# Kernel tuning notes

Measured on AMD Instinct MI355X. Metric: run time of the kernel, lower is better.

Reference implementation:

```python
import jax, jax.numpy as jnp
import numpy as np

CDIM = 256  # part_size for energy_pooling_mask


def setup_inputs() -> dict:
    key = jax.random.key(0)
    ks = jax.random.split(key, 6)
    B, T, IDIM, HDIM, ODIM = 8, 2048, 512, 2048, 512
    x = jax.random.normal(ks[0], (B, T, IDIM), dtype=jnp.float32)
    mask_prev = jax.random.randint(ks[1], (B, T, HDIM), 0, 2, dtype=jnp.int32)
    W_enc = jax.random.normal(ks[2], (HDIM, IDIM), dtype=jnp.float32) * 0.02
    b_enc = jax.random.normal(ks[3], (HDIM,), dtype=jnp.float32) * 0.02
    W_dec = jax.random.normal(ks[4], (ODIM, HDIM), dtype=jnp.float32) * 0.02
    b_dec = jax.random.normal(ks[5], (ODIM,), dtype=jnp.float32) * 0.02
    return {"x": x, "mask_prev": mask_prev, "W_enc": W_enc, "b_enc": b_enc,
            "W_dec": W_dec, "b_dec": b_dec}


def _energy_pooling_mask(h, part_size):
    # topk over channel (last) dim of h^2; share=True -> k = 2*part_size
    B, T, H = h.shape
    k2 = 2 * part_size
    _, idx = jax.lax.top_k(h * h, k2)            # [B, T, 2c] unique indices
    idx_f = idx.reshape(B * T, k2)
    rows = jnp.arange(B * T)[:, None]
    base = jnp.zeros((B * T, H), dtype=h.dtype)
    # sum of one-hots over unique indices == scatter-set of 1.0
    mask_share = base.at[rows, idx_f].set(1.0).reshape(B, T, H)
    mask_cur = base.at[rows, idx_f[:, :part_size]].set(1.0).reshape(B, T, H)
    return mask_cur, mask_share


def reference(x, mask_prev, W_enc, b_enc, W_dec, b_dec):
    # encoder: Linear(idim -> hdim)
    h = jnp.einsum('bti,hi->bth', x, W_enc) + b_enc
    # hidden_exclude_activation with mask_prev given:
    # h[mask_prev.bool()] = 0
    mp = mask_prev.astype(h.dtype)
    h = jnp.where(mp > 0, jnp.zeros((), h.dtype), h)
    mask_cur, mask_cur_share = _energy_pooling_mask(h, CDIM)
    mask_prev_new = mp + mask_cur
    # h.masked_fill(~mask_cur_share.bool(), 0)
    h = h * mask_cur_share
    # decoder_src: Linear(hdim -> odim)
    out = jnp.einsum('bth,oh->bto', h, W_dec) + b_dec
    return out, mask_prev_new
```

## Files before the change

### kernel.cpp

```cpp
#include <hip/hip_runtime.h>
#include <hip/hip_bf16.h>

typedef __attribute__((ext_vector_type(8))) __bf16 bf16x8;
typedef __attribute__((ext_vector_type(4))) float f32x4;

#define MDIM 16384
#define HDIM 2048
#define IDIM 512
#define ODIM 512
#define CAP 768

static __device__ __forceinline__ unsigned short f2bf(float f) {
  unsigned int u = __float_as_uint(f);
  unsigned int r = (u + 0x7fffu + ((u >> 16) & 1u)) >> 16;
  return (unsigned short)r;
}

__global__ void cvt_bf16_kernel(const float* __restrict__ src,
                                unsigned short* __restrict__ dst, int n) {
  int i = (blockIdx.x * 256 + threadIdx.x) * 4;
  if (i >= n) return;
  float4 v = *(const float4*)(src + i);
  unsigned int a = (unsigned int)f2bf(v.x) | ((unsigned int)f2bf(v.y) << 16);
  unsigned int b = (unsigned int)f2bf(v.z) | ((unsigned int)f2bf(v.w) << 16);
  uint2 st; st.x = a; st.y = b;
  *(uint2*)(dst + i) = st;
}

__global__ __launch_bounds__(256) void gemm1_kernel(
    const float* __restrict__ x,
    const float* __restrict__ wenc,
    const float* __restrict__ benc,
    float* __restrict__ h) {
  __shared__ __align__(16) float As[32][132];
  __shared__ __align__(16) float Bs[32][132];
  const int t = threadIdx.x;
  const int tx = t & 15, ty = t >> 4;
  const int m0 = blockIdx.y * 128;
  const int n0 = blockIdx.x * 128;
  const int r0 = t >> 1;
  const int kh = (t & 1) * 16;

  const float* pa = x + (size_t)(m0 + r0) * IDIM + kh;
  const float* pb = wenc + (size_t)(n0 + r0) * IDIM + kh;

  float acc[8][8];
#pragma unroll
  for (int i = 0; i < 8; ++i)
#pragma unroll
    for (int j = 0; j < 8; ++j) acc[i][j] = 0.f;

  for (int kt = 0; kt < IDIM; kt += 32) {
    float4 a0 = *(const float4*)(pa + kt);
    float4 a1 = *(const float4*)(pa + kt + 4);
    float4 a2 = *(const float4*)(pa + kt + 8);
    float4 a3 = *(const float4*)(pa + kt + 12);
    float4 b0 = *(const float4*)(pb + kt);
    float4 b1 = *(const float4*)(pb + kt + 4);
    float4 b2 = *(const float4*)(pb + kt + 8);
    float4 b3 = *(const float4*)(pb + kt + 12);
    __syncthreads();
    {
      const float* aa = (const float*)&a0;
      const float av[16] = {a0.x, a0.y, a0.z, a0.w, a1.x, a1.y, a1.z, a1.w,
                            a2.x, a2.y, a2.z, a2.w, a3.x, a3.y, a3.z, a3.w};
      const float bv[16] = {b0.x, b0.y, b0.z, b0.w, b1.x, b1.y, b1.z, b1.w,
                            b2.x, b2.y, b2.z, b2.w, b3.x, b3.y, b3.z, b3.w};
      (void)aa;
#pragma unroll
      for (int j = 0; j < 16; ++j) {
        As[kh + j][r0] = av[j];
        Bs[kh + j][r0] = bv[j];
      }
    }
    __syncthreads();
#pragma unroll
    for (int k = 0; k < 32; ++k) {
      float4 av0 = *(const float4*)&As[k][ty * 4];
      float4 av1 = *(const float4*)&As[k][64 + ty * 4];
      float4 bv0 = *(const float4*)&Bs[k][tx * 4];
      float4 bv1 = *(const float4*)&Bs[k][64 + tx * 4];
      float am[8] = {av0.x, av0.y, av0.z, av0.w, av1.x, av1.y, av1.z, av1.w};
      float bm[8] = {bv0.x, bv0.y, bv0.z, bv0.w, bv1.x, bv1.y, bv1.z, bv1.w};
#pragma unroll
      for (int i = 0; i < 8; ++i)
#pragma unroll
        for (int j = 0; j < 8; ++j) acc[i][j] += am[i] * bm[j];
    }
  }
  float4 be0 = *(const float4*)(benc + n0 + tx * 4);
  float4 be1 = *(const float4*)(benc + n0 + 64 + tx * 4);
  float bb[8] = {be0.x, be0.y, be0.z, be0.w, be1.x, be1.y, be1.z, be1.w};
#pragma unroll
  for (int i = 0; i < 8; ++i) {
    int m = m0 + ((i < 4) ? (ty * 4 + i) : (64 + ty * 4 + (i - 4)));
    float* hrow = h + (size_t)m * HDIM + n0;
    float4 s0 = {acc[i][0] + bb[0], acc[i][1] + bb[1], acc[i][2] + bb[2], acc[i][3] + bb[3]};
    float4 s1 = {acc[i][4] + bb[4], acc[i][5] + bb[5], acc[i][6] + bb[6], acc[i][7] + bb[7]};
    *(float4*)(hrow + tx * 4) = s0;
    *(float4*)(hrow + 64 + tx * 4) = s1;
  }
}

__global__ __launch_bounds__(256) void select_kernel(
    float* __restrict__ hbuf,
    const int* __restrict__ maskp,
    unsigned short* __restrict__ hs) {
  const int row = blockIdx.x;
  const int t = threadIdx.x;
  const int lane = t & 63;
  const int w = t >> 6;
  __shared__ int hist[4096];
  __shared__ unsigned int cand512[CAP];
  __shared__ unsigned int cand256[CAP];
  __shared__ int scal[16];
  __shared__ int n512, n256;

  float* hrow = hbuf + (size_t)row * HDIM;
  const int* mrow = maskp + (size_t)row * HDIM;
  float hv[8];
  *(float4*)&hv[0] = *(const float4*)(hrow + t * 8);
  *(float4*)&hv[4] = *(const float4*)(hrow + t * 8 + 4);
  int4 mp0 = *(const int4*)(mrow + t * 8);
  int4 mp1 = *(const int4*)(mrow + t * 8 + 4);
  int mm[8] = {mp0.x, mp0.y, mp0.z, mp0.w, mp1.x, mp1.y, mp1.z, mp1.w};
#pragma unroll
  for (int i = 0; i < 8; ++i) hv[i] = (mm[i] > 0) ? 0.f : hv[i];
  unsigned int key[8];
#pragma unroll
  for (int i = 0; i < 8; ++i) key[i] = __float_as_uint(hv[i] * hv[i]);

#pragma unroll
  for (int i = 0; i < 16; ++i) hist[t + i * 256] = 0;
  if (t == 0) {
    n512 = 0; n256 = 0;
    scal[0] = 0; scal[1] = 0x40000000;
    scal[2] = 0; scal[3] = 0x40000000;
  }
  __syncthreads();
#pragma unroll
  for (int i = 0; i < 8; ++i)
    if (key[i]) atomicAdd(&hist[key[i] >> 20], 1);
  __syncthreads();

  if (w == 0) {
    const int base = lane * 64;
    int s = 0;
#pragma unroll
    for (int i = 0; i < 64; i += 4) {
      int4 hh = *(const int4*)&hist[base + i];
      s += hh.x + hh.y + hh.z + hh.w;
    }
    int rs = s;
#pragma unroll
    for (int d = 1; d < 64; d <<= 1) {
      int o = __shfl_down(rs, d, 64);
      rs += (lane + d < 64) ? o : 0;
    }
    int c = rs - s;
    for (int i = 60; i >= 0; i -= 4) {
      int4 hh = *(const int4*)&hist[base + i];
      int q[4] = {hh.x, hh.y, hh.z, hh.w};
#pragma unroll
      for (int j = 3; j >= 0; --j) {
        int hc = q[j];
        if (c < 512 && c + hc >= 512) { scal[0] = base + i + j; scal[1] = 512 - c; }
        if (c < 256 && c + hc >= 256) { scal[2] = base + i + j; scal[3] = 256 - c; }
        c += hc;
      }
    }
  }
  __syncthreads();
  const int b512 = scal[0], b256 = scal[2];
#pragma unroll
  for (int i = 0; i < 8; ++i) {
    if (key[i]) {
      int bin = (int)(key[i] >> 20);
      if (bin == b512) { int p = atomicAdd(&n512, 1); if (p < CAP) cand512[p] = key[i]; }
      if (bin == b256) { int p = atomicAdd(&n256, 1); if (p < CAP) cand256[p] = key[i]; }
    }
  }
  __syncthreads();

  if (w < 2) {
    const unsigned int bb = (unsigned int)scal[w * 2];
    const int r = scal[w * 2 + 1];
    const unsigned int* cand = w ? cand256 : cand512;
    int C = w ? n256 : n512;
    C = (C < CAP) ? C : CAP;
    unsigned int v = 0;
    if (r <= C) {
      v = bb << 20;
      for (int bit = 19; bit >= 0; --bit) {
        unsigned int cth = v | (1u << bit);
        int cnt = 0;
        for (int p = lane; p < C; p += 64) cnt += (cand[p] >= cth) ? 1 : 0;
#pragma unroll
        for (int d = 1; d < 64; d <<= 1) cnt += __shfl_xor(cnt, d, 64);
        if (cnt >= r) v = cth;
      }
    }
    if (lane == 0) scal[4 + w] = (int)v;
  }
  __syncthreads();
  const unsigned int v512 = (unsigned int)scal[4];
  const unsigned int v256 = (unsigned int)scal[5];

  int g = 0;
#pragma unroll
  for (int i = 0; i < 8; ++i) {
    g += (key[i] > v512) ? 1 : 0;
    g += (key[i] > v256) ? (1 << 16) : 0;
  }
#pragma unroll
  for (int d = 1; d < 64; d <<= 1) g += __shfl_xor(g, d, 64);
  if (lane == 0) scal[8 + w] = g;
  __syncthreads();
  g = scal[8] + scal[9] + scal[10] + scal[11];
  const int r512 = 512 - (g & 0xffff);
  const int r256 = 256 - (g >> 16);

  int tc = 0;
#pragma unroll
  for (int i = 0; i < 8; ++i) {
    tc += (key[i] == v512) ? 1 : 0;
    tc += (key[i] == v256) ? (1 << 16) : 0;
  }
  int sc = tc;
#pragma unroll
  for (int d = 1; d < 64; d <<= 1) {
    int o = __shfl_up(sc, d, 64);
    if (lane >= d) sc += o;
  }
  if (lane == 63) scal[12 + w] = sc;
  __syncthreads();
  int excl = sc - tc;
  for (int i = 0; i < w; ++i) excl += scal[12 + i];
  int run512 = excl & 0xffff;
  int run256 = (excl >> 16) & 0xffff;

  float mpn[8];
  unsigned int hb[4];
#pragma unroll
  for (int i = 0; i < 8; ++i) {
    bool share, cur;
    if (key[i] > v512) share = true;
    else if (key[i] == v512) { share = (run512 < r512); run512++; }
    else share = false;
    if (key[i] > v256) cur = true;
    else if (key[i] == v256) { cur = (run256 < r256); run256++; }
    else cur = false;
    mpn[i] = (float)mm[i] + (cur ? 1.0f : 0.0f);
    unsigned short bbits = f2bf(share ? hv[i] : 0.0f);
    if (i & 1) hb[i >> 1] |= ((unsigned int)bbits << 16);
    else hb[i >> 1] = (unsigned int)bbits;
  }
  float4 s0 = {mpn[0], mpn[1], mpn[2], mpn[3]};
  float4 s1 = {mpn[4], mpn[5], mpn[6], mpn[7]};
  *(float4*)(hrow + t * 8) = s0;
  *(float4*)(hrow + t * 8 + 4) = s1;
  uint4 hstore = {hb[0], hb[1], hb[2], hb[3]};
  *(uint4*)(hs + (size_t)row * HDIM + t * 8) = hstore;
}

__global__ __launch_bounds__(256) void gemm2_kernel(
    const unsigned short* __restrict__ A,
    const unsigned short* __restrict__ B,
    const float* __restrict__ bdec,
    float* __restrict__ out) {
  __shared__ __align__(16) __bf16 As[64 * 32];
  __shared__ __align__(16) __bf16 Bs[128 * 32];
  const int t = threadIdx.x;
  const int lane = t & 63;
  const int w = t >> 6;
  const int wm = w >> 1, wn = w & 1;
  const int m0 = blockIdx.y * 64;
  const int n0 = blockIdx.x * 128;
  const int r = t >> 2;
  const int k8 = (t & 3) * 8;

  f32x4 acc[2][4];
#pragma unroll
  for (int i = 0; i < 2; ++i)
#pragma unroll
    for (int j = 0; j < 4; ++j) acc[i][j] = (f32x4){0.f, 0.f, 0.f, 0.f};

  const int la = lane & 15;
  const int kq = (lane >> 4) * 8;

  for (int kt = 0; kt < HDIM; kt += 32) {
    uint4 a0 = *(const uint4*)(A + (size_t)(m0 + r) * HDIM + kt + k8);
    uint4 b0 = *(const uint4*)(B + (size_t)(n0 + r) * HDIM + kt + k8);
    uint4 b1 = *(const uint4*)(B + (size_t)(n0 + 64 + r) * HDIM + kt + k8);
    __syncthreads();
    *(uint4*)&As[r * 32 + k8] = a0;
    *(uint4*)&Bs[r * 32 + k8] = b0;
    *(uint4*)&Bs[(64 + r) * 32 + k8] = b1;
    __syncthreads();
    bf16x8 af[2], bg[4];
#pragma unroll
    for (int mi = 0; mi < 2; ++mi)
      af[mi] = *(const bf16x8*)&As[(wm * 32 + mi * 16 + la) * 32 + kq];
#pragma unroll
    for (int ni = 0; ni < 4; ++ni)
      bg[ni] = *(const bf16x8*)&Bs[(wn * 64 + ni * 16 + la) * 32 + kq];
#pragma unroll
    for (int mi = 0; mi < 2; ++mi)
#pragma unroll
      for (int ni = 0; ni < 4; ++ni)
        acc[mi][ni] = __builtin_amdgcn_mfma_f32_16x16x32_bf16(
            af[mi], bg[ni], acc[mi][ni], 0, 0, 0);
  }
  const int rq = (lane >> 4) * 4;
#pragma unroll
  for (int mi = 0; mi < 2; ++mi) {
#pragma unroll
    for (int ni = 0; ni < 4; ++ni) {
      int n = n0 + wn * 64 + ni * 16 + la;
      float bd = bdec[n];
#pragma unroll
      for (int rr = 0; rr < 4; ++rr) {
        int m = m0 + wm * 32 + mi * 16 + rq + rr;
        out[(size_t)m * ODIM + n] = acc[mi][ni][rr] + bd;
      }
    }
  }
}

extern "C" void kernel_launch(void* const* d_in, const int* in_sizes, int n_in,
                              void* d_out, int out_size, void* d_ws, size_t ws_size,
                              hipStream_t stream) {
  const float* x = (const float*)d_in[0];
  const int* mask_prev = (const int*)d_in[1];
  const float* W_enc = (const float*)d_in[2];
  const float* b_enc = (const float*)d_in[3];
  const float* W_dec = (const float*)d_in[4];
  const float* b_dec = (const float*)d_in[5];

  float* out = (float*)d_out;
  float* hbuf = out + (size_t)MDIM * ODIM;
  unsigned short* hs = (unsigned short*)d_ws;
  unsigned short* wdec = hs + (size_t)MDIM * HDIM;

  cvt_bf16_kernel<<<dim3((ODIM * HDIM) / (256 * 4)), dim3(256), 0, stream>>>(
      W_dec, wdec, ODIM * HDIM);
  gemm1_kernel<<<dim3(HDIM / 128, MDIM / 128), dim3(256), 0, stream>>>(
      x, W_enc, b_enc, hbuf);
  select_kernel<<<dim3(MDIM), dim3(256), 0, stream>>>(hbuf, mask_prev, hs);
  gemm2_kernel<<<dim3(ODIM / 128, MDIM / 64), dim3(256), 0, stream>>>(
      hs, wdec, b_dec, out);
}
```

Baseline: 835.4 us.

## Enlarge gemm1 tile to 128x256 with 8x16 per-thread register blocking

The FP32 encoder GEMM tile grows from 128x128 to 128x256 and each thread now accumulates an 8x16 block instead of 8x8. The aim is more FMAs per shared-memory load and fewer blocks re-reading x. Each thread loads one full W_enc row segment for the B tile, and the inner loop is partially unrolled. The cost is 128 accumulator registers per thread plus operands, which with launch_bounds(256,2) risks register spills or lower occupancy.

```diff
diff --git a/kernel.cpp b/kernel.cpp
--- a/kernel.cpp
+++ b/kernel.cpp
@@ -27,28 +27,28 @@
   *(uint2*)(dst + i) = st;
 }
 
-__global__ __launch_bounds__(256) void gemm1_kernel(
+__global__ __launch_bounds__(256, 2) void gemm1_kernel(
     const float* __restrict__ x,
     const float* __restrict__ wenc,
     const float* __restrict__ benc,
     float* __restrict__ h) {
   __shared__ __align__(16) float As[32][132];
-  __shared__ __align__(16) float Bs[32][132];
+  __shared__ __align__(16) float Bs[32][260];
   const int t = threadIdx.x;
   const int tx = t & 15, ty = t >> 4;
   const int m0 = blockIdx.y * 128;
-  const int n0 = blockIdx.x * 128;
-  const int r0 = t >> 1;
+  const int n0 = blockIdx.x * 256;
+  const int rA = t >> 1;
   const int kh = (t & 1) * 16;
 
-  const float* pa = x + (size_t)(m0 + r0) * IDIM + kh;
-  const float* pb = wenc + (size_t)(n0 + r0) * IDIM + kh;
-
-  float acc[8][8];
+  const float* pa = x + (size_t)(m0 + rA) * IDIM + kh;
+  const float* pb = wenc + (size_t)(n0 + t) * IDIM;
+
+  float acc[8][16];
 #pragma unroll
   for (int i = 0; i < 8; ++i)
 #pragma unroll
-    for (int j = 0; j < 8; ++j) acc[i][j] = 0.f;
+    for (int j = 0; j < 16; ++j) acc[i][j] = 0.f;
 
   for (int kt = 0; kt < IDIM; kt += 32) {
     float4 a0 = *(const float4*)(pa + kt);
@@ -59,46 +59,59 @@
     float4 b1 = *(const float4*)(pb + kt + 4);
     float4 b2 = *(const float4*)(pb + kt + 8);
     float4 b3 = *(const float4*)(pb + kt + 12);
+    float4 b4 = *(const float4*)(pb + kt + 16);
+    float4 b5 = *(const float4*)(pb + kt + 20);
+    float4 b6 = *(const float4*)(pb + kt + 24);
+    float4 b7 = *(const float4*)(pb + kt + 28);
     __syncthreads();
     {
-      const float* aa = (const float*)&a0;
       const float av[16] = {a0.x, a0.y, a0.z, a0.w, a1.x, a1.y, a1.z, a1.w,
                             a2.x, a2.y, a2.z, a2.w, a3.x, a3.y, a3.z, a3.w};
-      const float bv[16] = {b0.x, b0.y, b0.z, b0.w, b1.x, b1.y, b1.z, b1.w,
-                            b2.x, b2.y, b2.z, b2.w, b3.x, b3.y, b3.z, b3.w};
-      (void)aa;
-#pragma unroll
-      for (int j = 0; j < 16; ++j) {
-        As[kh + j][r0] = av[j];
-        Bs[kh + j][r0] = bv[j];
-      }
+#pragma unroll
+      for (int j = 0; j < 16; ++j) As[kh + j][rA] = av[j];
+      const float bv[32] = {b0.x, b0.y, b0.z, b0.w, b1.x, b1.y, b1.z, b1.w,
+                            b2.x, b2.y, b2.z, b2.w, b3.x, b3.y, b3.z, b3.w,
+                            b4.x, b4.y, b4.z, b4.w, b5.x, b5.y, b5.z, b5.w,
+                            b6.x, b6.y, b6.z, b6.w, b7.x, b7.y, b7.z, b7.w};
+#pragma unroll
+      for (int j = 0; j < 32; ++j) Bs[j][t] = bv[j];
     }
     __syncthreads();
-#pragma unroll
+#pragma unroll 8
     for (int k = 0; k < 32; ++k) {
-      float4 av0 = *(const float4*)&As[k][ty * 4];
-      float4 av1 = *(const float4*)&As[k][64 + ty * 4];
-      float4 bv0 = *(const float4*)&Bs[k][tx * 4];
-      float4 bv1 = *(const float4*)&Bs[k][64 + tx * 4];
+      float4 av0 = *(const float4*)&As[k][ty * 8];
+      float4 av1 = *(const float4*)&As[k][ty * 8 + 4];
+      float4 bq0 = *(const float4*)&Bs[k][tx * 4];
+      float4 bq1 = *(const float4*)&Bs[k][64 + tx * 4];
+      float4 bq2 = *(const float4*)&Bs[k][128 + tx * 4];
+      float4 bq3 = *(const float4*)&Bs[k][192 + tx * 4];
       float am[8] = {av0.x, av0.y, av0.z, av0.w, av1.x, av1.y, av1.z, av1.w};
-      float bm[8] = {bv0.x, bv0.y, bv0.z, bv0.w, bv1.x, bv1.y, bv1.z, bv1.w};
+      float bm[16] = {bq0.x, bq0.y, bq0.z, bq0.w, bq1.x, bq1.y, bq1.z, bq1.w,
+                      bq2.x, bq2.y, bq2.z, bq2.w, bq3.x, bq3.y, bq3.z, bq3.w};
 #pragma unroll
       for (int i = 0; i < 8; ++i)
 #pragma unroll
-        for (int j = 0; j < 8; ++j) acc[i][j] += am[i] * bm[j];
+        for (int j = 0; j < 16; ++j) acc[i][j] += am[i] * bm[j];
     }
   }
   float4 be0 = *(const float4*)(benc + n0 + tx * 4);
   float4 be1 = *(const float4*)(benc + n0 + 64 + tx * 4);
-  float bb[8] = {be0.x, be0.y, be0.z, be0.w, be1.x, be1.y, be1.z, be1.w};
-#pragma unroll
-  for (int i = 0; i < 8; ++i) {
-    int m = m0 + ((i < 4) ? (ty * 4 + i) : (64 + ty * 4 + (i - 4)));
+  float4 be2 = *(const float4*)(benc + n0 + 128 + tx * 4);
+  float4 be3 = *(const float4*)(benc + n0 + 192 + tx * 4);
+  float bb[16] = {be0.x, be0.y, be0.z, be0.w, be1.x, be1.y, be1.z, be1.w,
+                  be2.x, be2.y, be2.z, be2.w, be3.x, be3.y, be3.z, be3.w};
+#pragma unroll
+  for (int i = 0; i < 8; ++i) {
+    int m = m0 + ty * 8 + i;
     float* hrow = h + (size_t)m * HDIM + n0;
-    float4 s0 = {acc[i][0] + bb[0], acc[i][1] + bb[1], acc[i][2] + bb[2], acc[i][3] + bb[3]};
-    float4 s1 = {acc[i][4] + bb[4], acc[i][5] + bb[5], acc[i][6] + bb[6], acc[i][7] + bb[7]};
-    *(float4*)(hrow + tx * 4) = s0;
-    *(float4*)(hrow + 64 + tx * 4) = s1;
+#pragma unroll
+    for (int q = 0; q < 4; ++q) {
+      float4 s = {acc[i][q * 4 + 0] + bb[q * 4 + 0],
+                  acc[i][q * 4 + 1] + bb[q * 4 + 1],
+                  acc[i][q * 4 + 2] + bb[q * 4 + 2],
+                  acc[i][q * 4 + 3] + bb[q * 4 + 3]};
+      *(float4*)(hrow + q * 64 + tx * 4) = s;
+    }
   }
 }
 
@@ -344,7 +357,7 @@
 
   cvt_bf16_kernel<<<dim3((ODIM * HDIM) / (256 * 4)), dim3(256), 0, stream>>>(
       W_dec, wdec, ODIM * HDIM);
-  gemm1_kernel<<<dim3(HDIM / 128, MDIM / 128), dim3(256), 0, stream>>>(
+  gemm1_kernel<<<dim3(HDIM / 256, MDIM / 128), dim3(256), 0, stream>>>(
       x, W_enc, b_enc, hbuf);
   select_kernel<<<dim3(MDIM), dim3(256), 0, stream>>>(hbuf, mask_prev, hs);
   gemm2_kernel<<<dim3(ODIM / 128, MDIM / 64), dim3(256), 0, stream>>>(
```

After: 848.8 us. Within noise of the previous version (+1.6%).

## Enlarge gemm2 tile to 128x128x64 with XOR-swizzled LDS layout

Applied to the files above, without the earlier changes.

The decoder GEMM block tile grows from 64x128 with K=32 to 128x128 with K=64, so each wave computes a 64x64 sub-tile with a 4x4 MFMA accumulator grid. Each K iteration does twice as many MFMAs per barrier pair and reuses each staged operand more. Shared-memory chunks are XOR-swizzled by row to avoid LDS bank conflicts on the fragment reads. Costs are higher register and LDS use (32KB per block), which may lower occupancy, and half as many blocks in the grid.

```diff
diff --git a/kernel.cpp b/kernel.cpp
--- a/kernel.cpp
+++ b/kernel.cpp
@@ -61,12 +61,10 @@
     float4 b3 = *(const float4*)(pb + kt + 12);
     __syncthreads();
     {
-      const float* aa = (const float*)&a0;
       const float av[16] = {a0.x, a0.y, a0.z, a0.w, a1.x, a1.y, a1.z, a1.w,
                             a2.x, a2.y, a2.z, a2.w, a3.x, a3.y, a3.z, a3.w};
       const float bv[16] = {b0.x, b0.y, b0.z, b0.w, b1.x, b1.y, b1.z, b1.w,
                             b2.x, b2.y, b2.z, b2.w, b3.x, b3.y, b3.z, b3.w};
-      (void)aa;
 #pragma unroll
       for (int j = 0; j < 16; ++j) {
         As[kh + j][r0] = av[j];
@@ -268,59 +266,80 @@
     const unsigned short* __restrict__ B,
     const float* __restrict__ bdec,
     float* __restrict__ out) {
-  __shared__ __align__(16) __bf16 As[64 * 32];
-  __shared__ __align__(16) __bf16 Bs[128 * 32];
+  __shared__ __align__(16) unsigned short As[128 * 64];
+  __shared__ __align__(16) unsigned short Bs[128 * 64];
   const int t = threadIdx.x;
   const int lane = t & 63;
   const int w = t >> 6;
   const int wm = w >> 1, wn = w & 1;
-  const int m0 = blockIdx.y * 64;
+  const int m0 = blockIdx.y * 128;
   const int n0 = blockIdx.x * 128;
-  const int r = t >> 2;
-  const int k8 = (t & 3) * 8;
-
-  f32x4 acc[2][4];
-#pragma unroll
-  for (int i = 0; i < 2; ++i)
+
+  f32x4 acc[4][4];
+#pragma unroll
+  for (int i = 0; i < 4; ++i)
 #pragma unroll
     for (int j = 0; j < 4; ++j) acc[i][j] = (f32x4){0.f, 0.f, 0.f, 0.f};
 
   const int la = lane & 15;
-  const int kq = (lane >> 4) * 8;
-
-  for (int kt = 0; kt < HDIM; kt += 32) {
-    uint4 a0 = *(const uint4*)(A + (size_t)(m0 + r) * HDIM + kt + k8);
-    uint4 b0 = *(const uint4*)(B + (size_t)(n0 + r) * HDIM + kt + k8);
-    uint4 b1 = *(const uint4*)(B + (size_t)(n0 + 64 + r) * HDIM + kt + k8);
+  const int kq = lane >> 4;
+
+  int srow[4], schunk[4];
+#pragma unroll
+  for (int i = 0; i < 4; ++i) {
+    int slot = i * 256 + t;
+    srow[i] = slot >> 3;
+    schunk[i] = (slot & 7) ^ (srow[i] & 7);
+  }
+
+  for (int kt = 0; kt < HDIM; kt += 64) {
+    uint4 av[4], bv[4];
+#pragma unroll
+    for (int i = 0; i < 4; ++i) {
+      av[i] = *(const uint4*)(A + (size_t)(m0 + srow[i]) * HDIM + kt + schunk[i] * 8);
+      bv[i] = *(const uint4*)(B + (size_t)(n0 + srow[i]) * HDIM + kt + schunk[i] * 8);
+    }
     __syncthreads();
-    *(uint4*)&As[r * 32 + k8] = a0;
-    *(uint4*)&Bs[r * 32 + k8] = b0;
-    *(uint4*)&Bs[(64 + r) * 32 + k8] = b1;
+#pragma unroll
+    for (int i = 0; i < 4; ++i) {
+      int slot = i * 256 + t;
+      *(uint4*)&As[slot * 8] = av[i];
+      *(uint4*)&Bs[slot * 8] = bv[i];
+    }
     __syncthreads();
-    bf16x8 af[2], bg[4];
-#pragma unroll
-    for (int mi = 0; mi < 2; ++mi)
-      af[mi] = *(const bf16x8*)&As[(wm * 32 + mi * 16 + la) * 32 + kq];
-#pragma unroll
-    for (int ni = 0; ni < 4; ++ni)
-      bg[ni] = *(const bf16x8*)&Bs[(wn * 64 + ni * 16 + la) * 32 + kq];
-#pragma unroll
-    for (int mi = 0; mi < 2; ++mi)
-#pragma unroll
-      for (int ni = 0; ni < 4; ++ni)
-        acc[mi][ni] = __builtin_amdgcn_mfma_f32_16x16x32_bf16(
-            af[mi], bg[ni], acc[mi][ni], 0, 0, 0);
+#pragma unroll
+    for (int kk = 0; kk < 2; ++kk) {
+      bf16x8 af[4], bg[4];
+#pragma unroll
+      for (int mi = 0; mi < 4; ++mi) {
+        int row = wm * 64 + mi * 16 + la;
+        int ch = (kk * 4 + kq) ^ (row & 7);
+        af[mi] = *(const bf16x8*)&As[row * 64 + ch * 8];
+      }
+#pragma unroll
+      for (int ni = 0; ni < 4; ++ni) {
+        int row = wn * 64 + ni * 16 + la;
+        int ch = (kk * 4 + kq) ^ (row & 7);
+        bg[ni] = *(const bf16x8*)&Bs[row * 64 + ch * 8];
+      }
+#pragma unroll
+      for (int mi = 0; mi < 4; ++mi)
+#pragma unroll
+        for (int ni = 0; ni < 4; ++ni)
+          acc[mi][ni] = __builtin_amdgcn_mfma_f32_16x16x32_bf16(
+              af[mi], bg[ni], acc[mi][ni], 0, 0, 0);
+    }
   }
   const int rq = (lane >> 4) * 4;
 #pragma unroll
-  for (int mi = 0; mi < 2; ++mi) {
+  for (int mi = 0; mi < 4; ++mi) {
 #pragma unroll
     for (int ni = 0; ni < 4; ++ni) {
       int n = n0 + wn * 64 + ni * 16 + la;
       float bd = bdec[n];
 #pragma unroll
       for (int rr = 0; rr < 4; ++rr) {
-        int m = m0 + wm * 32 + mi * 16 + rq + rr;
+        int m = m0 + wm * 64 + mi * 16 + rq + rr;
         out[(size_t)m * ODIM + n] = acc[mi][ni][rr] + bd;
       }
     }
@@ -347,6 +366,6 @@
   gemm1_kernel<<<dim3(HDIM / 128, MDIM / 128), dim3(256), 0, stream>>>(
       x, W_enc, b_enc, hbuf);
   select_kernel<<<dim3(MDIM), dim3(256), 0, stream>>>(hbuf, mask_prev, hs);
-  gemm2_kernel<<<dim3(ODIM / 128, MDIM / 64), dim3(256), 0, stream>>>(
+  gemm2_kernel<<<dim3(ODIM / 128, MDIM / 128), dim3(256), 0, stream>>>(
       hs, wdec, b_dec, out);
 }
```

Result: slower. 973.3 us (+16.5%).
